# Performance work log

Hardware: AMD Instinct MI355X
Metric: run time of the kernel (lower is better)

## Reference

```python
import jax, jax.numpy as jnp
import numpy as np

D_MODEL, D_STATE, EXPAND = 768, 16, 2
D_INNER = D_MODEL * EXPAND
B, L = 2, 2048


def setup_inputs() -> dict:
    key = jax.random.key(0)
    ks = jax.random.split(key, 10)
    s = 0.02  # init scale for projection weights
    return {
        "x": jax.random.normal(ks[0], (B, L, D_MODEL), jnp.float32),
        "in_w": jax.random.normal(ks[1], (D_MODEL, 2 * D_INNER), jnp.float32) * s,
        "conv_w": jax.random.normal(ks[2], (D_INNER, 1, 3), jnp.float32) * 0.1,
        "conv_b": jnp.zeros((D_INNER,), jnp.float32),
        "xproj_w": jax.random.normal(ks[3], (D_INNER, 2 * D_STATE), jnp.float32) * s,
        "dt_w": jax.random.normal(ks[4], (D_INNER, D_INNER), jnp.float32) * s,
        "dt_b": jnp.zeros((D_INNER,), jnp.float32),
        "A_log": jax.random.normal(ks[5], (D_INNER, D_STATE), jnp.float32) * 0.01,
        "D": jnp.ones((D_INNER,), jnp.float32),
        "out_w": jax.random.normal(ks[6], (D_INNER, D_MODEL), jnp.float32) * s,
    }


def reference(x, in_w, conv_w, conv_b, xproj_w, dt_w, dt_b, A_log, D, out_w):
    d_inner = conv_w.shape[0]
    d_state = A_log.shape[1]

    xz = x @ in_w                                   # [B,L,2*d_inner]
    x_c, z = jnp.split(xz, 2, axis=-1)

    # depthwise conv1d, kernel 3, padding 1
    xc = jnp.transpose(x_c, (0, 2, 1))              # [B,d_inner,L]
    xc = jax.lax.conv_general_dilated(
        xc, conv_w, window_strides=(1,), padding=[(1, 1)],
        feature_group_count=d_inner,
        dimension_numbers=("NCH", "OIH", "NCH"))
    xc = xc + conv_b[None, :, None]
    xc = jax.nn.silu(jnp.transpose(xc, (0, 2, 1)))  # [B,L,d_inner]

    Bs, Cs = jnp.split(xc @ xproj_w, 2, axis=-1)    # each [B,L,d_state]
    delta = jax.nn.softplus(xc @ dt_w + dt_b)       # [B,L,d_inner]
    A = -jnp.exp(A_log.astype(jnp.float32))         # [d_inner,d_state]

    deltaA = jnp.exp(jnp.einsum("bld,dn->bldn", delta, A))      # [B,L,d_inner,d_state]
    deltaBx = jnp.einsum("bld,bln->bldn", delta * xc, Bs)        # [B,L,d_inner,d_state]

    def step(h, inp):
        dA_t, dBx_t, c_t = inp                      # [B,d,n],[B,d,n],[B,n]
        h = dA_t * h + dBx_t
        y_t = jnp.einsum("bdn,bn->bd", h, c_t)
        return h, y_t

    h0 = jnp.zeros((x.shape[0], d_inner, d_state), xc.dtype)
    xs = (jnp.moveaxis(deltaA, 1, 0), jnp.moveaxis(deltaBx, 1, 0), jnp.moveaxis(Cs, 1, 0))
    _, ys = jax.lax.scan(step, h0, xs)              # ys: [L,B,d_inner]
    y = jnp.moveaxis(ys, 0, 1) + D * xc             # skip connection

    y = y * jax.nn.silu(z)
    return y @ out_w                                # [B,L,d_model]
```

## Files before the change

### kernel.cpp

```cpp
#include <hip/hip_runtime.h>
#include <cmath>

#define DMODEL 768
#define DINNER 1536
#define NSTATE 16
#define SEQL   2048
#define NCHUNK 32
#define CHLEN  64

#define DT_F32  0
#define DT_BF16 1
#define DT_ZERO 2

typedef __bf16 bf16x8 __attribute__((ext_vector_type(8)));
typedef float  f32x4  __attribute__((ext_vector_type(4)));

typedef __attribute__((address_space(3))) unsigned short lds_us;
typedef const __attribute__((address_space(1))) unsigned short glob_us;

__device__ __forceinline__ void async_cp16(glob_us* g, lds_us* l) {
    __builtin_amdgcn_global_load_lds((const __attribute__((address_space(1))) void*)g,
                                     (__attribute__((address_space(3))) void*)l, 16, 0, 0);
}

__device__ __forceinline__ float bf2f(unsigned short h) {
    union { unsigned u; float f; } v; v.u = ((unsigned)h) << 16; return v.f;
}
__device__ __forceinline__ unsigned short f2bf(float f) {
    union { float f; unsigned u; } v; v.f = f;
    unsigned r = (v.u + 0x7FFFu + ((v.u >> 16) & 1u)) >> 16;
    return (unsigned short)r;
}
__device__ int detect_dtype(const void* p) {
    const unsigned* u = (const unsigned*)p;
    int nzlo = 0, band = 0, anynz = 0;
    for (int i = 0; i < 64; ++i) {
        unsigned w = u[i];
        anynz |= (w != 0);
        unsigned lo = w & 0xFFFFu;
        if (lo) {
            ++nzlo;
            unsigned e8 = (lo >> 7) & 0xFF;
            if (e8 >= 0x60 && e8 <= 0x8E) ++band;
        }
    }
    if (nzlo >= 8) return (band * 2 > nzlo) ? DT_BF16 : DT_F32;
    return anynz ? DT_F32 : DT_ZERO;
}
__device__ __forceinline__ float LD(const void* p, size_t i, int dt) {
    if (dt == DT_BF16) return bf2f(((const unsigned short*)p)[i]);
    if (dt == DT_F32)  return ((const float*)p)[i];
    return 0.f;
}

__global__ __launch_bounds__(256) void prep_kernel(
    const void* __restrict__ x, const void* __restrict__ in_w,
    const void* __restrict__ cw, const void* __restrict__ cb,
    const void* __restrict__ xp, const void* __restrict__ dt_w,
    const void* __restrict__ db, const void* __restrict__ Al,
    const void* __restrict__ Dv, const void* __restrict__ out_w,
    unsigned short* __restrict__ xb, unsigned short* __restrict__ inT,
    unsigned short* __restrict__ dtT, unsigned short* __restrict__ outT,
    float* __restrict__ pf)
{
    __shared__ unsigned short tile[32][33];
    __shared__ int dts[6];
    const int blk = blockIdx.x;
    const int t   = threadIdx.x;

    if (blk < 324) {
        if (t == 0) {
            dts[0] = detect_dtype(cw); dts[1] = detect_dtype(cb);
            dts[2] = detect_dtype(db); dts[3] = detect_dtype(Al);
            dts[4] = detect_dtype(Dv); dts[5] = detect_dtype(xp);
        }
        __syncthreads();
        int g = blk * 256 + t;
        if (g >= 82944) return;
        const void* src; int local; int which;
        if      (g <  4608) { src = cw; local = g;         which = 0; }
        else if (g <  6144) { src = cb; local = g - 4608;  which = 1; }
        else if (g <  7680) { src = db; local = g - 6144;  which = 2; }
        else if (g < 32256) { src = Al; local = g - 7680;  which = 3; }
        else if (g < 33792) { src = Dv; local = g - 32256; which = 4; }
        else                { src = xp; local = g - 33792; which = 5; }
        pf[g] = LD(src, local, dts[which]);
    } else if (blk < 3396) {
        if (t == 0) dts[0] = detect_dtype(x);
        __syncthreads();
        const int dt = dts[0];
        size_t i = ((size_t)(blk - 324) * 256 + t) * 4;
        ushort4 o;
        o.x = f2bf(LD(x, i + 0, dt)); o.y = f2bf(LD(x, i + 1, dt));
        o.z = f2bf(LD(x, i + 2, dt)); o.w = f2bf(LD(x, i + 3, dt));
        *(ushort4*)&xb[i] = o;
    } else {
        const void* src; unsigned short* dst; int R, C, tx_n, idx;
        if (blk < 5700)      { src = in_w;  dst = inT;  R = 768;  C = 3072; tx_n = 96; idx = blk - 3396; }
        else if (blk < 8004) { src = dt_w;  dst = dtT;  R = 1536; C = 1536; tx_n = 48; idx = blk - 5700; }
        else                 { src = out_w; dst = outT; R = 1536; C = 768;  tx_n = 24; idx = blk - 8004; }
        if (t == 0) dts[0] = detect_dtype(src);
        __syncthreads();
        const int dt = dts[0];
        const int tx = t & 31, ty = t >> 5;
        const int bx = (idx % tx_n) * 32, by = (idx / tx_n) * 32;
        #pragma unroll
        for (int i = 0; i < 4; ++i) {
            int r = by + ty + i * 8;
            tile[ty + i * 8][tx] = f2bf(LD(src, (size_t)r * C + bx + tx, dt));
        }
        __syncthreads();
        #pragma unroll
        for (int i = 0; i < 4; ++i) {
            int c = bx + ty + i * 8;
            dst[(size_t)c * R + by + tx] = tile[tx][ty + i * 8];
        }
    }
}

template<int EPI>
__global__ __launch_bounds__(256) void gemm_kernel(
    const unsigned short* __restrict__ A, const unsigned short* __restrict__ Bt,
    void* __restrict__ C0, void* __restrict__ C1, const float* __restrict__ biasf,
    int M, int N, int K)
{
    __shared__ __align__(16) unsigned short As[2][128 * 32];
    __shared__ __align__(16) unsigned short Bs[2][64 * 32];
    const int t    = threadIdx.x;
    const int m0   = blockIdx.x * 128;
    const int n0   = blockIdx.y * 64;
    const int w    = t >> 6;
    const int lane = t & 63;
    const int wm   = (w >> 1) * 64, wn = (w & 1) * 32;
    const int lm   = lane & 15, quad = lane >> 4;
    const int srow = lane >> 2;
    const int sg   = lane & 3;

    f32x4 acc[4][2] = {};

    #pragma unroll
    for (int h = 0; h < 2; ++h) {
        int row = w * 32 + h * 16 + srow;
        int kg  = (sg - (row >> 1)) & 3;
        async_cp16((glob_us*)&A[(size_t)(m0 + row) * K + kg * 8],
                   (lds_us*)&As[0][(w * 32 + h * 16) * 32]);
    }
    {
        int brow = w * 16 + srow;
        int bkg  = (sg - (brow >> 1)) & 3;
        async_cp16((glob_us*)&Bt[(size_t)(n0 + brow) * K + bkg * 8],
                   (lds_us*)&Bs[0][(w * 16) * 32]);
    }

    int p = 0;
    for (int k0 = 0; k0 < K; k0 += 32) {
        __syncthreads();
        if (k0 + 32 < K) {
            #pragma unroll
            for (int h = 0; h < 2; ++h) {
                int row = w * 32 + h * 16 + srow;
                int kg  = (sg - (row >> 1)) & 3;
                async_cp16((glob_us*)&A[(size_t)(m0 + row) * K + k0 + 32 + kg * 8],
                           (lds_us*)&As[p ^ 1][(w * 32 + h * 16) * 32]);
            }
            int brow = w * 16 + srow;
            int bkg  = (sg - (brow >> 1)) & 3;
            async_cp16((glob_us*)&Bt[(size_t)(n0 + brow) * K + k0 + 32 + bkg * 8],
                       (lds_us*)&Bs[p ^ 1][(w * 16) * 32]);
        }
        bf16x8 af[4], bfr[2];
        #pragma unroll
        for (int i = 0; i < 4; ++i) {
            int row = wm + i * 16 + lm;
            int g   = (quad + (row >> 1)) & 3;
            af[i] = *(const bf16x8*)&As[p][row * 32 + g * 8];
        }
        #pragma unroll
        for (int j = 0; j < 2; ++j) {
            int row = wn + j * 16 + lm;
            int g   = (quad + (row >> 1)) & 3;
            bfr[j] = *(const bf16x8*)&Bs[p][row * 32 + g * 8];
        }
        #pragma unroll
        for (int i = 0; i < 4; ++i)
            #pragma unroll
            for (int j = 0; j < 2; ++j)
                acc[i][j] = __builtin_amdgcn_mfma_f32_16x16x32_bf16(af[i], bfr[j], acc[i][j], 0, 0, 0);
        p ^= 1;
    }

    const int half = N >> 1;
    #pragma unroll
    for (int i = 0; i < 4; ++i) {
        #pragma unroll
        for (int j = 0; j < 2; ++j) {
            int col = n0 + wn + j * 16 + lm;
            #pragma unroll
            for (int r = 0; r < 4; ++r) {
                int row = m0 + wm + i * 16 + quad * 4 + r;
                float v = acc[i][j][r];
                if (EPI == 1) {
                    v += biasf[col];
                    float sp = (v > 20.f) ? v : log1pf(__expf(v));
                    ((unsigned short*)C0)[(size_t)row * N + col] = f2bf(sp);
                } else if (EPI == 2) {
                    ((float*)C0)[(size_t)row * N + col] = v;
                } else {
                    if (col < half) {
                        ((unsigned short*)C0)[(size_t)row * half + col] = f2bf(v);
                    } else {
                        float s = v / (1.f + __expf(-v));
                        ((unsigned short*)C1)[(size_t)row * half + col - half] = f2bf(s);
                    }
                }
            }
        }
    }
}

__global__ __launch_bounds__(256) void conv_silu_kernel(
    const unsigned short* __restrict__ xcpre, const float* __restrict__ cwf,
    const float* __restrict__ cbf, unsigned short* __restrict__ xcb)
{
    int idx = blockIdx.x * 256 + threadIdx.x;
    int d   = idx % DINNER;
    int row = idx / DINNER;
    int l   = row % SEQL;
    size_t base = (size_t)row * DINNER + d;
    float acc = cbf[d];
    if (l > 0)        acc += bf2f(xcpre[base - DINNER]) * cwf[d * 3 + 0];
    acc += bf2f(xcpre[base]) * cwf[d * 3 + 1];
    if (l < SEQL - 1) acc += bf2f(xcpre[base + DINNER]) * cwf[d * 3 + 2];
    float s = acc / (1.f + __expf(-acc));
    xcb[base] = f2bf(s);
}

__global__ __launch_bounds__(128) void xproj_kernel(
    const unsigned short* __restrict__ xcb, const float* __restrict__ wf,
    float* __restrict__ BC)
{
    __shared__ float red[4][32][4];
    const int t = threadIdx.x;
    const int s = t & 31, part = t >> 5;
    const int row0 = blockIdx.x * 4;
    float acc[4] = {0.f, 0.f, 0.f, 0.f};
    for (int k = part * 384; k < (part + 1) * 384; ++k) {
        float wv = wf[k * 32 + s];
        #pragma unroll
        for (int r = 0; r < 4; ++r)
            acc[r] += bf2f(xcb[(size_t)(row0 + r) * DINNER + k]) * wv;
    }
    #pragma unroll
    for (int r = 0; r < 4; ++r) red[part][s][r] = acc[r];
    __syncthreads();
    if (t < 32) {
        #pragma unroll
        for (int r = 0; r < 4; ++r)
            BC[(size_t)(row0 + r) * 32 + t] =
                red[0][t][r] + red[1][t][r] + red[2][t][r] + red[3][t][r];
    }
}

__global__ __launch_bounds__(256) void scan_phase_a(
    const unsigned short* __restrict__ dlt, const unsigned short* __restrict__ xcb,
    const float* __restrict__ BC, const float* __restrict__ A_log_f,
    unsigned short* __restrict__ P, float* __restrict__ S)
{
    int g = blockIdx.x * 256 + threadIdx.x;
    int d = g % DINNER;
    int c = (g / DINNER) % NCHUNK;
    int b = g / (DINNER * NCHUNK);
    f32x4 A4[4], h4[4];
    const f32x4* al4 = (const f32x4*)&A_log_f[d * 16];
    #pragma unroll
    for (int q = 0; q < 4; ++q) {
        f32x4 al = al4[q];
        f32x4 a;
        a[0] = -__expf(al[0]); a[1] = -__expf(al[1]);
        a[2] = -__expf(al[2]); a[3] = -__expf(al[3]);
        A4[q] = a;
        h4[q] = (f32x4){0.f, 0.f, 0.f, 0.f};
    }
    float sdv = 0.f;
    const int row0 = b * SEQL + c * CHLEN;
    for (int l = 0; l < CHLEN; ++l) {
        size_t row = (size_t)(row0 + l);
        float dv = bf2f(dlt[row * DINNER + d]);
        float xv = bf2f(xcb[row * DINNER + d]);
        float dx = dv * xv;
        sdv += dv;
        const f32x4* bc4 = (const f32x4*)&BC[row * 32];
        #pragma unroll
        for (int q = 0; q < 4; ++q) {
            f32x4 Bq = bc4[q];
            f32x4 e;
            e[0] = __expf(dv * A4[q][0]); e[1] = __expf(dv * A4[q][1]);
            e[2] = __expf(dv * A4[q][2]); e[3] = __expf(dv * A4[q][3]);
            h4[q] = e * h4[q] + dx * Bq;
        }
    }
    size_t idx = (((size_t)(b * NCHUNK + c)) * DINNER + d) * 16;
    #pragma unroll
    for (int q = 0; q < 4; ++q) {
        *(f32x4*)&S[idx + q * 4] = h4[q];
        ushort4 pq;
        pq.x = f2bf(__expf(sdv * A4[q][0]));
        pq.y = f2bf(__expf(sdv * A4[q][1]));
        pq.z = f2bf(__expf(sdv * A4[q][2]));
        pq.w = f2bf(__expf(sdv * A4[q][3]));
        *(ushort4*)&P[idx + q * 4] = pq;
    }
}

__global__ __launch_bounds__(256) void scan_combine(
    const unsigned short* __restrict__ P, float* __restrict__ S)
{
    int t = blockIdx.x * 256 + threadIdx.x;
    int b = t / (DINNER * NSTATE);
    int dn = t % (DINNER * NSTATE);
    float H = 0.f;
    for (int c = 0; c < NCHUNK; ++c) {
        size_t idx = ((size_t)(b * NCHUNK + c)) * (DINNER * NSTATE) + dn;
        float Pv = bf2f(P[idx]);
        float Sv = S[idx];
        S[idx] = H;
        H = Pv * H + Sv;
    }
}

__global__ __launch_bounds__(256) void scan_phase_c(
    const unsigned short* __restrict__ dlt, const unsigned short* __restrict__ xcb,
    const float* __restrict__ BC, const unsigned short* __restrict__ zg,
    const float* __restrict__ A_log_f, const float* __restrict__ D_f,
    const float* __restrict__ Hin, unsigned short* __restrict__ yg)
{
    int g = blockIdx.x * 256 + threadIdx.x;
    int d = g % DINNER;
    int c = (g / DINNER) % NCHUNK;
    int b = g / (DINNER * NCHUNK);
    f32x4 A4[4], h4[4];
    const f32x4* al4 = (const f32x4*)&A_log_f[d * 16];
    size_t hidx = (((size_t)(b * NCHUNK + c)) * DINNER + d) * 16;
    const f32x4* hin4 = (const f32x4*)&Hin[hidx];
    #pragma unroll
    for (int q = 0; q < 4; ++q) {
        f32x4 al = al4[q];
        f32x4 a;
        a[0] = -__expf(al[0]); a[1] = -__expf(al[1]);
        a[2] = -__expf(al[2]); a[3] = -__expf(al[3]);
        A4[q] = a;
        h4[q] = hin4[q];
    }
    const float Dd = D_f[d];
    const int row0 = b * SEQL + c * CHLEN;
    for (int l = 0; l < CHLEN; ++l) {
        size_t row = (size_t)(row0 + l);
        float dv = bf2f(dlt[row * DINNER + d]);
        float xv = bf2f(xcb[row * DINNER + d]);
        float zv = bf2f(zg[row * DINNER + d]);
        float dx = dv * xv;
        const f32x4* bc4 = (const f32x4*)&BC[row * 32];
        f32x4 yv = (f32x4){0.f, 0.f, 0.f, 0.f};
        #pragma unroll
        for (int q = 0; q < 4; ++q) {
            f32x4 Bq = bc4[q];
            f32x4 Cq = bc4[4 + q];
            f32x4 e;
            e[0] = __expf(dv * A4[q][0]); e[1] = __expf(dv * A4[q][1]);
            e[2] = __expf(dv * A4[q][2]); e[3] = __expf(dv * A4[q][3]);
            h4[q] = e * h4[q] + dx * Bq;
            yv = yv + h4[q] * Cq;
        }
        float y = yv[0] + yv[1] + yv[2] + yv[3];
        yg[row * DINNER + d] = f2bf((y + Dd * xv) * zv);
    }
}

__global__ void guard_kernel(float* out, int code)
{
    if (threadIdx.x == 0 && blockIdx.x == 0 && code) out[0] = (float)code;
}

extern "C" void kernel_launch(void* const* d_in, const int* in_sizes, int n_in,
                              void* d_out, int out_size, void* d_ws, size_t ws_size,
                              hipStream_t stream) {
    static const int EXPECTED[10] = {3145728, 2359296, 4608, 1536, 49152,
                                     2359296, 1536, 24576, 1536, 1179648};
    bool ok = (n_in == 10);
    if (ok) for (int i = 0; i < 10; ++i) ok = ok && (in_sizes[i] == EXPECTED[i]);
    int code = 0;
    if (!ok) code = 2000;
    else if (ws_size < 67895296ULL) code = 3000;
    if (code) { guard_kernel<<<1, 64, 0, stream>>>((float*)d_out, code); return; }

    const void* x       = d_in[0];
    const void* in_w    = d_in[1];
    const void* conv_w  = d_in[2];
    const void* conv_b  = d_in[3];
    const void* xproj_w = d_in[4];
    const void* dt_w    = d_in[5];
    const void* dt_b    = d_in[6];
    const void* A_log   = d_in[7];
    const void* Dvec    = d_in[8];
    const void* out_w   = d_in[9];

    char* ws = (char*)d_ws;
    float* conv_w_f = (float*)(ws + 0);
    float* conv_b_f = (float*)(ws + 18432);
    float* dt_b_f   = (float*)(ws + 24576);
    float* A_log_f  = (float*)(ws + 30720);
    float* D_f      = (float*)(ws + 129024);
    float* xproj_f  = (float*)(ws + 135168);
    unsigned short* xb    = (unsigned short*)(ws + 524288);
    unsigned short* inT   = (unsigned short*)(ws + 6815744);
    unsigned short* yg    = (unsigned short*)(ws + 524288);
    unsigned short* dtT   = (unsigned short*)(ws + 13107200);
    unsigned short* outT  = (unsigned short*)(ws + 17825792);
    unsigned short* xcpre = (unsigned short*)(ws + 20185088);
    unsigned short* dlt   = xcpre;
    float*          BC    = (float*)(ws + 32768000);
    unsigned short* zg    = (unsigned short*)(ws + 33292288);
    unsigned short* xcb   = (unsigned short*)(ws + 45875200);
    float*          scanS = (float*)(ws + 58458112);
    unsigned short* scanP = (unsigned short*)(ws + 64749568);

    prep_kernel<<<9156, 256, 0, stream>>>(x, in_w, conv_w, conv_b, xproj_w, dt_w,
                                          dt_b, A_log, Dvec, out_w,
                                          xb, inT, dtT, outT, (float*)ws);

    gemm_kernel<3><<<dim3(32, 48), 256, 0, stream>>>(xb, inT, (void*)xcpre, (void*)zg,
                                                     nullptr, 4096, 3072, 768);
    conv_silu_kernel<<<(4096 * DINNER) / 256, 256, 0, stream>>>(xcpre, conv_w_f, conv_b_f, xcb);
    xproj_kernel<<<1024, 128, 0, stream>>>(xcb, xproj_f, BC);
    gemm_kernel<1><<<dim3(32, 24), 256, 0, stream>>>(xcb, dtT, (void*)dlt, nullptr,
                                                     dt_b_f, 4096, 1536, 1536);
    scan_phase_a<<<384, 256, 0, stream>>>(dlt, xcb, BC, A_log_f, scanP, scanS);
    scan_combine<<<192, 256, 0, stream>>>(scanP, scanS);
    scan_phase_c<<<384, 256, 0, stream>>>(dlt, xcb, BC, zg, A_log_f, D_f, scanS, yg);
    gemm_kernel<2><<<dim3(32, 12), 256, 0, stream>>>(yg, outT, d_out, nullptr,
                                                    nullptr, 4096, 768, 1536);
}
```

Before: 369.3 us.

## Triple-buffer GEMM LDS tiles with partial vmcnt waits to deepen prefetch

The bf16 MFMA GEMM now keeps three LDS stages instead of two and issues loads two k-tiles ahead. Each iteration waits with s_waitcnt vmcnt(3) instead of draining every load, so the newest tile can stay in flight while the current one is computed. Global pointers are precomputed once and the loop is split into stage/compute lambdas. This uses more LDS per block, which may lower occupancy, and correctness now depends on the manual waitcnt counting.

```diff
diff --git a/kernel.cpp b/kernel.cpp
--- a/kernel.cpp
+++ b/kernel.cpp
@@ -124,8 +124,8 @@
     void* __restrict__ C0, void* __restrict__ C1, const float* __restrict__ biasf,
     int M, int N, int K)
 {
-    __shared__ __align__(16) unsigned short As[2][128 * 32];
-    __shared__ __align__(16) unsigned short Bs[2][64 * 32];
+    __shared__ __align__(16) unsigned short As[3][128 * 32];
+    __shared__ __align__(16) unsigned short Bs[3][64 * 32];
     const int t    = threadIdx.x;
     const int m0   = blockIdx.x * 128;
     const int n0   = blockIdx.y * 64;
@@ -136,58 +136,60 @@
     const int srow = lane >> 2;
     const int sg   = lane & 3;
 
+    const int arow0 = w * 32 + srow;
+    const int arow1 = w * 32 + 16 + srow;
+    const int akg0  = (sg - (arow0 >> 1)) & 3;
+    const int akg1  = (sg - (arow1 >> 1)) & 3;
+    const int brow  = w * 16 + srow;
+    const int bkg   = (sg - (brow >> 1)) & 3;
+    glob_us* gA0 = (glob_us*)&A[(size_t)(m0 + arow0) * K + akg0 * 8];
+    glob_us* gA1 = (glob_us*)&A[(size_t)(m0 + arow1) * K + akg1 * 8];
+    glob_us* gB  = (glob_us*)&Bt[(size_t)(n0 + brow) * K + bkg * 8];
+
     f32x4 acc[4][2] = {};
-
-    #pragma unroll
-    for (int h = 0; h < 2; ++h) {
-        int row = w * 32 + h * 16 + srow;
-        int kg  = (sg - (row >> 1)) & 3;
-        async_cp16((glob_us*)&A[(size_t)(m0 + row) * K + kg * 8],
-                   (lds_us*)&As[0][(w * 32 + h * 16) * 32]);
-    }
-    {
-        int brow = w * 16 + srow;
-        int bkg  = (sg - (brow >> 1)) & 3;
-        async_cp16((glob_us*)&Bt[(size_t)(n0 + brow) * K + bkg * 8],
-                   (lds_us*)&Bs[0][(w * 16) * 32]);
-    }
-
-    int p = 0;
-    for (int k0 = 0; k0 < K; k0 += 32) {
-        __syncthreads();
-        if (k0 + 32 < K) {
-            #pragma unroll
-            for (int h = 0; h < 2; ++h) {
-                int row = w * 32 + h * 16 + srow;
-                int kg  = (sg - (row >> 1)) & 3;
-                async_cp16((glob_us*)&A[(size_t)(m0 + row) * K + k0 + 32 + kg * 8],
-                           (lds_us*)&As[p ^ 1][(w * 32 + h * 16) * 32]);
-            }
-            int brow = w * 16 + srow;
-            int bkg  = (sg - (brow >> 1)) & 3;
-            async_cp16((glob_us*)&Bt[(size_t)(n0 + brow) * K + k0 + 32 + bkg * 8],
-                       (lds_us*)&Bs[p ^ 1][(w * 16) * 32]);
-        }
+    const int nt = K >> 5;
+
+    auto stage = [&](int tt, int q) {
+        int k0 = tt * 32;
+        async_cp16(gA0 + k0, (lds_us*)&As[q][(w * 32) * 32]);
+        async_cp16(gA1 + k0, (lds_us*)&As[q][(w * 32 + 16) * 32]);
+        async_cp16(gB  + k0, (lds_us*)&Bs[q][(w * 16) * 32]);
+    };
+    auto compute = [&](int q) {
         bf16x8 af[4], bfr[2];
         #pragma unroll
         for (int i = 0; i < 4; ++i) {
             int row = wm + i * 16 + lm;
             int g   = (quad + (row >> 1)) & 3;
-            af[i] = *(const bf16x8*)&As[p][row * 32 + g * 8];
+            af[i] = *(const bf16x8*)&As[q][row * 32 + g * 8];
         }
         #pragma unroll
         for (int j = 0; j < 2; ++j) {
             int row = wn + j * 16 + lm;
             int g   = (quad + (row >> 1)) & 3;
-            bfr[j] = *(const bf16x8*)&Bs[p][row * 32 + g * 8];
+            bfr[j] = *(const bf16x8*)&Bs[q][row * 32 + g * 8];
         }
         #pragma unroll
         for (int i = 0; i < 4; ++i)
             #pragma unroll
             for (int j = 0; j < 2; ++j)
                 acc[i][j] = __builtin_amdgcn_mfma_f32_16x16x32_bf16(af[i], bfr[j], acc[i][j], 0, 0, 0);
-        p ^= 1;
-    }
+    };
+
+    stage(0, 0);
+    stage(1, 1);
+
+    for (int tt = 0; tt < nt - 1; ++tt) {
+        asm volatile("s_waitcnt vmcnt(3)" ::: "memory");
+        __builtin_amdgcn_s_barrier();
+        __builtin_amdgcn_sched_barrier(0);
+        if (tt + 2 < nt) stage(tt + 2, (tt + 2) % 3);
+        compute(tt % 3);
+    }
+    asm volatile("s_waitcnt vmcnt(0)" ::: "memory");
+    __builtin_amdgcn_s_barrier();
+    __builtin_amdgcn_sched_barrier(0);
+    compute((nt - 1) % 3);
 
     const int half = N >> 1;
     #pragma unroll
```

Measured after the change: 376.2 us. About the same (+1.9%).

## Split scan state dimension across four lanes per channel to raise parallelism

Applied to the files above, without the earlier changes.

The chunked scan phase-A and phase-C kernels now assign four threads per (batch, chunk, channel), each owning four of the sixteen state elements, instead of one thread handling all sixteen. Grids grow fourfold. Phase C reduces the partial C-dot products with two xor shuffles, and lane 0 applies the z gate and writes the output. This raises occupancy and latency hiding in scan kernels that previously launched only 384 blocks, at the cost of redundant delta/x loads across the four lanes and extra shuffles.

```diff
diff --git a/kernel.cpp b/kernel.cpp
--- a/kernel.cpp
+++ b/kernel.cpp
@@ -267,20 +267,15 @@
     unsigned short* __restrict__ P, float* __restrict__ S)
 {
     int g = blockIdx.x * 256 + threadIdx.x;
-    int d = g % DINNER;
-    int c = (g / DINNER) % NCHUNK;
-    int b = g / (DINNER * NCHUNK);
-    f32x4 A4[4], h4[4];
-    const f32x4* al4 = (const f32x4*)&A_log_f[d * 16];
-    #pragma unroll
-    for (int q = 0; q < 4; ++q) {
-        f32x4 al = al4[q];
-        f32x4 a;
-        a[0] = -__expf(al[0]); a[1] = -__expf(al[1]);
-        a[2] = -__expf(al[2]); a[3] = -__expf(al[3]);
-        A4[q] = a;
-        h4[q] = (f32x4){0.f, 0.f, 0.f, 0.f};
-    }
+    int q = g & 3;
+    int d = (g >> 2) % DINNER;
+    int c = ((g >> 2) / DINNER) % NCHUNK;
+    int b = (g >> 2) / (DINNER * NCHUNK);
+    f32x4 al = *(const f32x4*)&A_log_f[d * 16 + q * 4];
+    f32x4 A1;
+    A1[0] = -__expf(al[0]); A1[1] = -__expf(al[1]);
+    A1[2] = -__expf(al[2]); A1[3] = -__expf(al[3]);
+    f32x4 h = (f32x4){0.f, 0.f, 0.f, 0.f};
     float sdv = 0.f;
     const int row0 = b * SEQL + c * CHLEN;
     for (int l = 0; l < CHLEN; ++l) {
@@ -289,27 +284,20 @@
         float xv = bf2f(xcb[row * DINNER + d]);
         float dx = dv * xv;
         sdv += dv;
-        const f32x4* bc4 = (const f32x4*)&BC[row * 32];
-        #pragma unroll
-        for (int q = 0; q < 4; ++q) {
-            f32x4 Bq = bc4[q];
-            f32x4 e;
-            e[0] = __expf(dv * A4[q][0]); e[1] = __expf(dv * A4[q][1]);
-            e[2] = __expf(dv * A4[q][2]); e[3] = __expf(dv * A4[q][3]);
-            h4[q] = e * h4[q] + dx * Bq;
-        }
-    }
-    size_t idx = (((size_t)(b * NCHUNK + c)) * DINNER + d) * 16;
-    #pragma unroll
-    for (int q = 0; q < 4; ++q) {
-        *(f32x4*)&S[idx + q * 4] = h4[q];
-        ushort4 pq;
-        pq.x = f2bf(__expf(sdv * A4[q][0]));
-        pq.y = f2bf(__expf(sdv * A4[q][1]));
-        pq.z = f2bf(__expf(sdv * A4[q][2]));
-        pq.w = f2bf(__expf(sdv * A4[q][3]));
-        *(ushort4*)&P[idx + q * 4] = pq;
-    }
+        f32x4 Bq = *(const f32x4*)&BC[row * 32 + q * 4];
+        f32x4 e;
+        e[0] = __expf(dv * A1[0]); e[1] = __expf(dv * A1[1]);
+        e[2] = __expf(dv * A1[2]); e[3] = __expf(dv * A1[3]);
+        h = e * h + dx * Bq;
+    }
+    size_t idx = (((size_t)(b * NCHUNK + c)) * DINNER + d) * 16 + q * 4;
+    *(f32x4*)&S[idx] = h;
+    ushort4 pq;
+    pq.x = f2bf(__expf(sdv * A1[0]));
+    pq.y = f2bf(__expf(sdv * A1[1]));
+    pq.z = f2bf(__expf(sdv * A1[2]));
+    pq.w = f2bf(__expf(sdv * A1[3]));
+    *(ushort4*)&P[idx] = pq;
 }
 
 __global__ __launch_bounds__(256) void scan_combine(
@@ -335,44 +323,37 @@
     const float* __restrict__ Hin, unsigned short* __restrict__ yg)
 {
     int g = blockIdx.x * 256 + threadIdx.x;
-    int d = g % DINNER;
-    int c = (g / DINNER) % NCHUNK;
-    int b = g / (DINNER * NCHUNK);
-    f32x4 A4[4], h4[4];
-    const f32x4* al4 = (const f32x4*)&A_log_f[d * 16];
-    size_t hidx = (((size_t)(b * NCHUNK + c)) * DINNER + d) * 16;
-    const f32x4* hin4 = (const f32x4*)&Hin[hidx];
-    #pragma unroll
-    for (int q = 0; q < 4; ++q) {
-        f32x4 al = al4[q];
-        f32x4 a;
-        a[0] = -__expf(al[0]); a[1] = -__expf(al[1]);
-        a[2] = -__expf(al[2]); a[3] = -__expf(al[3]);
-        A4[q] = a;
-        h4[q] = hin4[q];
-    }
+    int q = g & 3;
+    int d = (g >> 2) % DINNER;
+    int c = ((g >> 2) / DINNER) % NCHUNK;
+    int b = (g >> 2) / (DINNER * NCHUNK);
+    f32x4 al = *(const f32x4*)&A_log_f[d * 16 + q * 4];
+    f32x4 A1;
+    A1[0] = -__expf(al[0]); A1[1] = -__expf(al[1]);
+    A1[2] = -__expf(al[2]); A1[3] = -__expf(al[3]);
+    size_t hidx = (((size_t)(b * NCHUNK + c)) * DINNER + d) * 16 + q * 4;
+    f32x4 h = *(const f32x4*)&Hin[hidx];
     const float Dd = D_f[d];
     const int row0 = b * SEQL + c * CHLEN;
     for (int l = 0; l < CHLEN; ++l) {
         size_t row = (size_t)(row0 + l);
         float dv = bf2f(dlt[row * DINNER + d]);
         float xv = bf2f(xcb[row * DINNER + d]);
-        float zv = bf2f(zg[row * DINNER + d]);
         float dx = dv * xv;
-        const f32x4* bc4 = (const f32x4*)&BC[row * 32];
-        f32x4 yv = (f32x4){0.f, 0.f, 0.f, 0.f};
-        #pragma unroll
-        for (int q = 0; q < 4; ++q) {
-            f32x4 Bq = bc4[q];
-            f32x4 Cq = bc4[4 + q];
-            f32x4 e;
-            e[0] = __expf(dv * A4[q][0]); e[1] = __expf(dv * A4[q][1]);
-            e[2] = __expf(dv * A4[q][2]); e[3] = __expf(dv * A4[q][3]);
-            h4[q] = e * h4[q] + dx * Bq;
-            yv = yv + h4[q] * Cq;
-        }
+        f32x4 Bq = *(const f32x4*)&BC[row * 32 + q * 4];
+        f32x4 Cq = *(const f32x4*)&BC[row * 32 + 16 + q * 4];
+        f32x4 e;
+        e[0] = __expf(dv * A1[0]); e[1] = __expf(dv * A1[1]);
+        e[2] = __expf(dv * A1[2]); e[3] = __expf(dv * A1[3]);
+        h = e * h + dx * Bq;
+        f32x4 yv = h * Cq;
         float y = yv[0] + yv[1] + yv[2] + yv[3];
-        yg[row * DINNER + d] = f2bf((y + Dd * xv) * zv);
+        y += __shfl_xor(y, 1);
+        y += __shfl_xor(y, 2);
+        if (q == 0) {
+            float zv = bf2f(zg[row * DINNER + d]);
+            yg[row * DINNER + d] = f2bf((y + Dd * xv) * zv);
+        }
     }
 }
 
@@ -434,9 +415,9 @@
     xproj_kernel<<<1024, 128, 0, stream>>>(xcb, xproj_f, BC);
     gemm_kernel<1><<<dim3(32, 24), 256, 0, stream>>>(xcb, dtT, (void*)dlt, nullptr,
                                                      dt_b_f, 4096, 1536, 1536);
-    scan_phase_a<<<384, 256, 0, stream>>>(dlt, xcb, BC, A_log_f, scanP, scanS);
+    scan_phase_a<<<1536, 256, 0, stream>>>(dlt, xcb, BC, A_log_f, scanP, scanS);
     scan_combine<<<192, 256, 0, stream>>>(scanP, scanS);
-    scan_phase_c<<<384, 256, 0, stream>>>(dlt, xcb, BC, zg, A_log_f, D_f, scanS, yg);
+    scan_phase_c<<<1536, 256, 0, stream>>>(dlt, xcb, BC, zg, A_log_f, D_f, scanS, yg);
     gemm_kernel<2><<<dim3(32, 12), 256, 0, stream>>>(yg, outT, d_out, nullptr,
                                                     nullptr, 4096, 768, 1536);
 }
```

Result: faster. 357.5 us (-3.2%).
